# Kernel optimization log

Measured on AMD Instinct MI355X. Metric: run time of the kernel, lower is better.

## Reference

```python
import jax, jax.numpy as jnp
import numpy as np

B, D, NT, NZ = 16384, 64, 128, 2048


def setup_inputs() -> dict:
    key = jax.random.key(0)
    ks = jax.random.split(key, 5)
    return {
        "t": jax.random.uniform(ks[0], (1,), dtype=jnp.float32),
        "z": jax.random.normal(ks[1], (B, D), dtype=jnp.float32),
        "logp_z": jnp.zeros((B, 1), jnp.float32),
        "centres_z": jax.random.normal(ks[2], (NZ, D), dtype=jnp.float32),
        "log_sigmas_z": jnp.zeros((NZ,), jnp.float32),
        "centres_t": jax.random.normal(ks[3], (NT, 1), dtype=jnp.float32),
        "log_sigmas_t": jnp.zeros((NT,), jnp.float32),
        "W": 0.01 * jax.random.normal(ks[4], (D, NT, NZ + 1), dtype=jnp.float32),
    }


def _gauss(r):
    return jnp.exp(-r * r)


def _forward(t, z, centres_z, log_sigmas_z, centres_t, log_sigmas_t, W):
    # time RBF features Phi_t: (NT,)
    r_t = jnp.abs(t.reshape(1, 1) - centres_t.reshape(1, -1)) / jnp.exp(log_sigmas_t)
    phi_t = _gauss(r_t).reshape(-1)
    W_t = jnp.einsum('dij,i->dj', W, phi_t)  # (D, NZ+1)
    Wz, bias = W_t[:, :-1], W_t[:, -1]       # bias comes from the appended ones column
    # z RBF features via squared-distance identity (avoids [B,NZ,D] blowup)
    sq = (jnp.sum(z * z, axis=1, keepdims=True)
          + jnp.sum(centres_z * centres_z, axis=1)[None, :]
          - 2.0 * z @ centres_z.T)
    sq = jnp.maximum(sq, 0.0)                 # (B, NZ) squared distances
    inv_s2 = jnp.exp(-2.0 * log_sigmas_z)     # 1/sigma_j^2, (NZ,)
    phi_z = jnp.exp(-sq * inv_s2)             # gaussian(||z-c_j||/s_j), (B, NZ)
    dz_dt = phi_z @ Wz.T + bias               # (B, D)
    # exact Jacobian trace for gaussian basis:
    #   d phi_j / d z_i = -2 * phi_j * (z_i - c_{j,i}) / s_j^2
    #   tr(J)_b = sum_j phi_{b,j} * inv_s2_j * (-2) * (sum_i Wz[i,j] z_{b,i} - sum_i Wz[i,j] c_{j,i})
    q = jnp.einsum('dj,jd->j', Wz, centres_z)  # (NZ,)
    trace = -2.0 * jnp.sum(phi_z * inv_s2 * (z @ Wz - q), axis=1)  # (B,)
    dlogp_z_dt = -trace[:, None]               # (B, 1)
    return dz_dt, dlogp_z_dt


def reference(t, z, logp_z, centres_z, log_sigmas_z, centres_t, log_sigmas_t, W):
    return _forward(t, z, centres_z, log_sigmas_z, centres_t, log_sigmas_t, W)
```

## Files before the change

### kernel.cpp

```cpp
#include <hip/hip_runtime.h>
#include <math.h>

typedef unsigned int uint;
typedef unsigned short ushort;
typedef unsigned char uchar;
typedef unsigned long ulong_;
typedef __attribute__((ext_vector_type(4))) float f32x4;

#define BB  16384
#define DD  64
#define NT_ 128
#define NZ_ 2048
#define NJ_ 2049

#define BIAS_OFF 0
#define SCS_OFF  64
#define CZ8A_OFF 8256
#define CZ8B_OFF 24640
#define WZ8A_OFF 41024
#define WZ8B_OFF 57408
#define WZBP_OFF 73792
#define PART_OFF 106560

#if __has_builtin(__builtin_amdgcn_cvt_pk_fp8_f32)
__device__ __forceinline__ uint pk4_fp8(float a, float b, float c, float d) {
  int v = __builtin_amdgcn_cvt_pk_fp8_f32(a, b, 0, false);
  v = __builtin_amdgcn_cvt_pk_fp8_f32(c, d, v, true);
  return (uint)v;
}
__device__ __forceinline__ uchar f8_1(float x) {
  return (uchar)(__builtin_amdgcn_cvt_pk_fp8_f32(x, x, 0, false) & 0xFF);
}
#else
__device__ __forceinline__ uint sw_f8(float x) {
  uint u = __float_as_uint(x);
  uint s = (u >> 24) & 0x80u;
  float ax = __uint_as_float(u & 0x7FFFFFFFu);
  if (!(ax >= 0.015625f)) return s;
  if (ax >= 448.f) return s | 0x7Eu;
  uint q = __float_as_uint(ax);
  q += 0x7FFFFu + ((q >> 20) & 1u);
  uint e = (q >> 23) - 120u;
  return s | ((e & 0xFu) << 3) | ((q >> 20) & 7u);
}
__device__ __forceinline__ uchar f8_1(float x) { return (uchar)sw_f8(x); }
__device__ __forceinline__ uint pk4_fp8(float a, float b, float c, float d) {
  return sw_f8(a) | (sw_f8(b) << 8) | (sw_f8(c) << 16) | (sw_f8(d) << 24);
}
#endif

__global__ __launch_bounds__(256) void k_wt1(
    const float* __restrict__ t, const float* __restrict__ ct,
    const float* __restrict__ lst, const float* __restrict__ W,
    float* __restrict__ part)
{
  __shared__ float ph[32];
  int tx = threadIdx.x;
  int d  = blockIdx.y;
  int ic = blockIdx.z;
  if (tx < 32) {
    int i = ic * 32 + tx;
    float r = fabsf(t[0] - ct[i]) * __expf(-lst[i]);
    ph[tx] = __expf(-r * r);
  }
  __syncthreads();
  int j = blockIdx.x * 256 + tx;
  if (j >= NJ_) return;
  const float* Wp = W + (size_t)d * NT_ * NJ_ + (size_t)(ic * 32) * NJ_ + j;
  float acc = 0.f;
#pragma unroll
  for (int k = 0; k < 32; ++k) acc += Wp[(size_t)k * NJ_] * ph[k];
  part[((size_t)ic * 64 + d) * NJ_ + j] = acc;
}

__global__ __launch_bounds__(256) void k_prep2(
    const float* __restrict__ part, const float* __restrict__ cz,
    const float* __restrict__ lsz,
    float* __restrict__ bias, float4* __restrict__ scs,
    uchar* __restrict__ cz8a, uchar* __restrict__ cz8b,
    uchar* __restrict__ wz8a, uchar* __restrict__ wz8b,
    uchar* __restrict__ wzbp8)
{
  __shared__ float wt[64][9];
  int tid = threadIdx.x;
  int cb0 = blockIdx.x * 8;
#pragma unroll
  for (int h = 0; h < 2; ++h) {
    int f = h * 256 + tid;
    int d = f >> 3, c = f & 7;
    size_t idx = (size_t)d * NJ_ + cb0 + c;
    float s = part[idx] + part[(size_t)64 * NJ_ + idx]
            + part[(size_t)128 * NJ_ + idx] + part[(size_t)192 * NJ_ + idx];
    wt[d][c] = s;
    int cg = cb0 + c;
    wzbp8[((size_t)(cg >> 5) * 64 + d) * 32 + (cg & 31)] = f8_1(s);
  }
  if (blockIdx.x == 0 && tid < 64) {
    size_t idx = (size_t)tid * NJ_ + 2048;
    bias[tid] = part[idx] + part[(size_t)64 * NJ_ + idx]
              + part[(size_t)128 * NJ_ + idx] + part[(size_t)192 * NJ_ + idx];
  }
  __syncthreads();
  int cl = tid >> 5;
  int k  = tid & 31;
  int c  = cb0 + cl;
  float cv0 = cz[(size_t)c * DD + k];
  float cv1 = cz[(size_t)c * DD + 32 + k];
  cz8a[(size_t)c * 32 + k] = f8_1(cv0);
  cz8b[(size_t)c * 32 + k] = f8_1(cv1);
  float w0 = wt[k][cl], w1 = wt[32 + k][cl];
  wz8a[(size_t)c * 32 + k] = f8_1(w0);
  wz8b[(size_t)c * 32 + k] = f8_1(w1);
  float ca = cv0 * cv0 + cv1 * cv1;
  float qa = w0 * cv0 + w1 * cv1;
  qa += __shfl_xor(qa, 1);  ca += __shfl_xor(ca, 1);
  qa += __shfl_xor(qa, 2);  ca += __shfl_xor(ca, 2);
  qa += __shfl_xor(qa, 4);  ca += __shfl_xor(ca, 4);
  qa += __shfl_xor(qa, 8);  ca += __shfl_xor(ca, 8);
  qa += __shfl_xor(qa, 16); ca += __shfl_xor(ca, 16);
  if (k == 0) {
    float inv = __expf(-2.f * lsz[c]);
    scs[c] = make_float4(ca, inv, qa, inv * 1.44269504f);
  }
}

#define PH_LD 40

__global__ __launch_bounds__(256, 2) void k_fused(
    const float* __restrict__ z,
    const uchar* __restrict__ cz8a, const uchar* __restrict__ cz8b,
    const uchar* __restrict__ wz8a, const uchar* __restrict__ wz8b,
    const uchar* __restrict__ wzbp8,
    const float4* __restrict__ scs, const float* __restrict__ bias,
    float* __restrict__ out)
{
  __shared__ char smem[10240];
  __shared__ float dlr[4][32];
  uchar* phs = (uchar*)smem;
  float* eps = (float*)smem;

  int tid  = threadIdx.x;
  int ws   = tid >> 6;
  int lane = tid & 63;
  int lrow = lane & 15, quad = lane >> 4;
  int b0 = blockIdx.x * 32;

  long az[2][2];
  float zzr[2][4];
#pragma unroll
  for (int mt = 0; mt < 2; ++mt) {
    const float* zr = z + (size_t)(b0 + mt * 16 + lrow) * DD + quad * 8;
    float4 v0 = *(const float4*)zr;
    float4 v1 = *(const float4*)(zr + 4);
    float4 v2 = *(const float4*)(zr + 32);
    float4 v3 = *(const float4*)(zr + 36);
    uint l0 = pk4_fp8(v0.x, v0.y, v0.z, v0.w);
    uint l1 = pk4_fp8(v1.x, v1.y, v1.z, v1.w);
    uint h0 = pk4_fp8(v2.x, v2.y, v2.z, v2.w);
    uint h1 = pk4_fp8(v3.x, v3.y, v3.z, v3.w);
    az[mt][0] = (long)(((ulong_)l1 << 32) | l0);
    az[mt][1] = (long)(((ulong_)h1 << 32) | h0);
    float ss = v0.x * v0.x + v0.y * v0.y + v0.z * v0.z + v0.w * v0.w
             + v1.x * v1.x + v1.y * v1.y + v1.z * v1.z + v1.w * v1.w
             + v2.x * v2.x + v2.y * v2.y + v2.z * v2.z + v2.w * v2.w
             + v3.x * v3.x + v3.y * v3.y + v3.z * v3.z + v3.w * v3.w;
    ss += __shfl_xor(ss, 16);
    ss += __shfl_xor(ss, 32);
#pragma unroll
    for (int i = 0; i < 4; ++i) zzr[mt][i] = __shfl(ss, quad * 4 + i);
  }

  f32x4 acc[2][4];
#pragma unroll
  for (int mt = 0; mt < 2; ++mt)
#pragma unroll
    for (int nt = 0; nt < 4; ++nt) acc[mt][nt] = (f32x4){0.f, 0.f, 0.f, 0.f};
  float dl[2][4] = {{0.f}};

  const f32x4 zero = (f32x4){0.f, 0.f, 0.f, 0.f};
  int cbase = ws * 512;
  int pbase = ws * 32 * PH_LD;

  long Abc0[2][2], Abc1[2][2], Abw0[2][2], Abw1[2][2], Abb[2][4];
  float4 Asc[2][2];
#define LOADB(PAR, C0)                                                         \
  do {                                                                         \
    int c0_ = (C0);                                                            \
    _Pragma("unroll")                                                          \
    for (int nt = 0; nt < 2; ++nt) {                                           \
      int cg_ = c0_ + nt * 16 + lrow;                                          \
      size_t ro_ = (size_t)cg_ * 32 + quad * 8;                                \
      Abc0[PAR][nt] = *(const long*)(cz8a + ro_);                              \
      Abc1[PAR][nt] = *(const long*)(cz8b + ro_);                              \
      Abw0[PAR][nt] = *(const long*)(wz8a + ro_);                              \
      Abw1[PAR][nt] = *(const long*)(wz8b + ro_);                              \
      Asc[PAR][nt]  = scs[cg_];                                                \
    }                                                                          \
    size_t cb_ = (size_t)(c0_ >> 5) * 64 * 32;                                 \
    _Pragma("unroll")                                                          \
    for (int nt = 0; nt < 4; ++nt)                                             \
      Abb[PAR][nt] =                                                           \
          *(const long*)(wzbp8 + cb_ + (size_t)(nt * 16 + lrow) * 32 + quad * 8); \
  } while (0)

  LOADB(0, cbase);
#pragma unroll 2
  for (int it = 0; it < 16; ++it) {
    int par = it & 1;
    int pb = par * (4 * 32 * PH_LD) + pbase;

    f32x4 d1a[2][2], d2a[2][2];
#pragma unroll
    for (int nt = 0; nt < 2; ++nt)
#pragma unroll
      for (int mt = 0; mt < 2; ++mt) {
        f32x4 d1 = __builtin_amdgcn_mfma_f32_16x16x32_fp8_fp8(az[mt][0], Abc0[par][nt], zero, 0, 0, 0);
        d1       = __builtin_amdgcn_mfma_f32_16x16x32_fp8_fp8(az[mt][1], Abc1[par][nt], d1,   0, 0, 0);
        f32x4 d2 = __builtin_amdgcn_mfma_f32_16x16x32_fp8_fp8(az[mt][0], Abw0[par][nt], zero, 0, 0, 0);
        d2       = __builtin_amdgcn_mfma_f32_16x16x32_fp8_fp8(az[mt][1], Abw1[par][nt], d2,   0, 0, 0);
        d1a[nt][mt] = d1;
        d2a[nt][mt] = d2;
      }

    LOADB(par ^ 1, cbase + ((it + 1) & 15) * 32);

#pragma unroll
    for (int nt = 0; nt < 2; ++nt) {
      float4 sc = Asc[par][nt];
#pragma unroll
      for (int mt = 0; mt < 2; ++mt) {
#pragma unroll
        for (int i = 0; i < 4; ++i) {
          float e = fmaf(d1a[nt][mt][i], 2.f, -(zzr[mt][i] + sc.x)) * sc.w;
          e = fminf(e, 0.f);
          float p;
          asm("v_exp_f32 %0, %1" : "=v"(p) : "v"(e));
          dl[mt][i] += p * sc.y * (d2a[nt][mt][i] - sc.z);
          phs[pb + (mt * 16 + quad * 4 + i) * PH_LD + nt * 16 + lrow] = f8_1(p);
        }
      }
    }

    long ap0 = *(const long*)&phs[pb + lrow * PH_LD + quad * 8];
    long ap1 = *(const long*)&phs[pb + (16 + lrow) * PH_LD + quad * 8];
    __builtin_amdgcn_s_setprio(1);
#pragma unroll
    for (int nt = 0; nt < 4; ++nt) {
      acc[0][nt] = __builtin_amdgcn_mfma_f32_16x16x32_fp8_fp8(ap0, Abb[par][nt], acc[0][nt], 0, 0, 0);
      acc[1][nt] = __builtin_amdgcn_mfma_f32_16x16x32_fp8_fp8(ap1, Abb[par][nt], acc[1][nt], 0, 0, 0);
    }
    __builtin_amdgcn_s_setprio(0);
  }
#undef LOADB

#pragma unroll
  for (int mt = 0; mt < 2; ++mt)
#pragma unroll
    for (int i = 0; i < 4; ++i) {
      float v = dl[mt][i];
      v += __shfl_xor(v, 1);
      v += __shfl_xor(v, 2);
      v += __shfl_xor(v, 4);
      v += __shfl_xor(v, 8);
      if (lrow == 0) dlr[ws][mt * 16 + quad * 4 + i] = v;
    }

  for (int s = 0; s < 4; ++s) {
    __syncthreads();
    if (ws == s) {
#pragma unroll
      for (int mt = 0; mt < 2; ++mt)
#pragma unroll
        for (int nt = 0; nt < 4; ++nt)
#pragma unroll
          for (int i = 0; i < 4; ++i) {
            int r = mt * 16 + quad * 4 + i;
            int d = nt * 16 + lrow;
            if (s == 0) eps[r * 68 + d] = acc[mt][nt][i];
            else        eps[r * 68 + d] += acc[mt][nt][i];
          }
    }
  }
  __syncthreads();

  {
    int r = tid >> 3, d0 = (tid & 7) * 8;
    float4 e0 = *(const float4*)&eps[r * 68 + d0];
    float4 e1 = *(const float4*)&eps[r * 68 + d0 + 4];
    float4 bv0 = *(const float4*)&bias[d0];
    float4 bv1 = *(const float4*)&bias[d0 + 4];
    float4 o0, o1;
    o0.x = e0.x + bv0.x; o0.y = e0.y + bv0.y; o0.z = e0.z + bv0.z; o0.w = e0.w + bv0.w;
    o1.x = e1.x + bv1.x; o1.y = e1.y + bv1.y; o1.z = e1.z + bv1.z; o1.w = e1.w + bv1.w;
    *(float4*)&out[(size_t)(b0 + r) * DD + d0]     = o0;
    *(float4*)&out[(size_t)(b0 + r) * DD + d0 + 4] = o1;
  }
  if (tid < 32) {
    float s = dlr[0][tid] + dlr[1][tid] + dlr[2][tid] + dlr[3][tid];
    out[(size_t)BB * DD + b0 + tid] = 2.f * s;
  }
}

extern "C" void kernel_launch(void* const* d_in, const int* in_sizes, int n_in,
                              void* d_out, int out_size, void* d_ws, size_t ws_size,
                              hipStream_t stream)
{
  const float* t   = (const float*)d_in[0];
  const float* z   = (const float*)d_in[1];
  const float* cz  = (const float*)d_in[3];
  const float* lsz = (const float*)d_in[4];
  const float* ct  = (const float*)d_in[5];
  const float* lst = (const float*)d_in[6];
  const float* W   = (const float*)d_in[7];
  float* out = (float*)d_out;
  float* ws  = (float*)d_ws;

  float*  bias = ws + BIAS_OFF;
  float4* scs  = (float4*)(ws + SCS_OFF);
  uchar*  cz8a = (uchar*)(ws + CZ8A_OFF);
  uchar*  cz8b = (uchar*)(ws + CZ8B_OFF);
  uchar*  wz8a = (uchar*)(ws + WZ8A_OFF);
  uchar*  wz8b = (uchar*)(ws + WZ8B_OFF);
  uchar*  wzbp8 = (uchar*)(ws + WZBP_OFF);
  float*  part = ws + PART_OFF;

  k_wt1<<<dim3(9, 64, 4), 256, 0, stream>>>(t, ct, lst, W, part);
  k_prep2<<<dim3(256), 256, 0, stream>>>(part, cz, lsz, bias, scs,
                                         cz8a, cz8b, wz8a, wz8b, wzbp8);
  k_fused<<<dim3(BB / 32), 256, 0, stream>>>(z, cz8a, cz8b,
                                             wz8a, wz8b, wzbp8, scs, bias, out);
}
```

Measured before the change: 137.8 us.

## Transpose MFMA operands so phi stays in registers, replacing LDS staging with shuffles

The first-stage MFMAs now take the centre/weight tiles as the A operand and z as B, so each lane's results run along centres for a single batch row. The fp8 phi tile for the second MFMA is then built from packed registers with cross-lane shuffles instead of being written to and read back from shared memory. Per-centre constants are split into separate float arrays, loaded as float4 along the centre axis and pre-folded (−c²·il2, −inv·q), which trims the per-element arithmetic and the trace reduction. The cost is extra shuffle and select instructions plus three global float4 loads per iteration.

```diff
diff --git a/kernel.cpp b/kernel.cpp
--- a/kernel.cpp
+++ b/kernel.cpp
@@ -14,13 +14,15 @@
 #define NJ_ 2049
 
 #define BIAS_OFF 0
-#define SCS_OFF  64
-#define CZ8A_OFF 8256
-#define CZ8B_OFF 24640
-#define WZ8A_OFF 41024
-#define WZ8B_OFF 57408
-#define WZBP_OFF 73792
-#define PART_OFF 106560
+#define IL2_OFF  64
+#define A0_OFF   2112
+#define NIQ_OFF  4160
+#define CZ8A_OFF 6208
+#define CZ8B_OFF 22592
+#define WZ8A_OFF 38976
+#define WZ8B_OFF 55360
+#define WZBP_OFF 71744
+#define PART_OFF 104512
 
 #if __has_builtin(__builtin_amdgcn_cvt_pk_fp8_f32)
 __device__ __forceinline__ uint pk4_fp8(float a, float b, float c, float d) {
@@ -76,7 +78,8 @@
 __global__ __launch_bounds__(256) void k_prep2(
     const float* __restrict__ part, const float* __restrict__ cz,
     const float* __restrict__ lsz,
-    float* __restrict__ bias, float4* __restrict__ scs,
+    float* __restrict__ bias,
+    float* __restrict__ il2a, float* __restrict__ a0a, float* __restrict__ niqa,
     uchar* __restrict__ cz8a, uchar* __restrict__ cz8b,
     uchar* __restrict__ wz8a, uchar* __restrict__ wz8b,
     uchar* __restrict__ wzbp8)
@@ -120,24 +123,24 @@
   qa += __shfl_xor(qa, 16); ca += __shfl_xor(ca, 16);
   if (k == 0) {
     float inv = __expf(-2.f * lsz[c]);
-    scs[c] = make_float4(ca, inv, qa, inv * 1.44269504f);
-  }
-}
-
-#define PH_LD 40
+    float il2 = inv * 1.44269504f;
+    il2a[c] = il2;
+    a0a[c]  = -ca * il2;
+    niqa[c] = -inv * qa;
+  }
+}
 
 __global__ __launch_bounds__(256, 2) void k_fused(
     const float* __restrict__ z,
     const uchar* __restrict__ cz8a, const uchar* __restrict__ cz8b,
     const uchar* __restrict__ wz8a, const uchar* __restrict__ wz8b,
     const uchar* __restrict__ wzbp8,
-    const float4* __restrict__ scs, const float* __restrict__ bias,
-    float* __restrict__ out)
+    const float* __restrict__ il2a, const float* __restrict__ a0a,
+    const float* __restrict__ niqa,
+    const float* __restrict__ bias, float* __restrict__ out)
 {
-  __shared__ char smem[10240];
+  __shared__ float eps[32 * 68];
   __shared__ float dlr[4][32];
-  uchar* phs = (uchar*)smem;
-  float* eps = (float*)smem;
 
   int tid  = threadIdx.x;
   int ws   = tid >> 6;
@@ -146,7 +149,7 @@
   int b0 = blockIdx.x * 32;
 
   long az[2][2];
-  float zzr[2][4];
+  float nzz[2];
 #pragma unroll
   for (int mt = 0; mt < 2; ++mt) {
     const float* zr = z + (size_t)(b0 + mt * 16 + lrow) * DD + quad * 8;
@@ -166,8 +169,7 @@
              + v3.x * v3.x + v3.y * v3.y + v3.z * v3.z + v3.w * v3.w;
     ss += __shfl_xor(ss, 16);
     ss += __shfl_xor(ss, 32);
-#pragma unroll
-    for (int i = 0; i < 4; ++i) zzr[mt][i] = __shfl(ss, quad * 4 + i);
+    nzz[mt] = -ss;
   }
 
   f32x4 acc[2][4];
@@ -175,14 +177,12 @@
   for (int mt = 0; mt < 2; ++mt)
 #pragma unroll
     for (int nt = 0; nt < 4; ++nt) acc[mt][nt] = (f32x4){0.f, 0.f, 0.f, 0.f};
-  float dl[2][4] = {{0.f}};
+  float dl[2] = {0.f, 0.f};
 
   const f32x4 zero = (f32x4){0.f, 0.f, 0.f, 0.f};
   int cbase = ws * 512;
-  int pbase = ws * 32 * PH_LD;
 
   long Abc0[2][2], Abc1[2][2], Abw0[2][2], Abw1[2][2], Abb[2][4];
-  float4 Asc[2][2];
 #define LOADB(PAR, C0)                                                         \
   do {                                                                         \
     int c0_ = (C0);                                                            \
@@ -194,7 +194,6 @@
       Abc1[PAR][nt] = *(const long*)(cz8b + ro_);                              \
       Abw0[PAR][nt] = *(const long*)(wz8a + ro_);                              \
       Abw1[PAR][nt] = *(const long*)(wz8b + ro_);                              \
-      Asc[PAR][nt]  = scs[cg_];                                                \
     }                                                                          \
     size_t cb_ = (size_t)(c0_ >> 5) * 64 * 32;                                 \
     _Pragma("unroll")                                                          \
@@ -207,42 +206,67 @@
 #pragma unroll 2
   for (int it = 0; it < 16; ++it) {
     int par = it & 1;
-    int pb = par * (4 * 32 * PH_LD) + pbase;
+    int c0  = cbase + it * 32;
+
+    float4 ilv[2], a0v[2], nqv[2];
+#pragma unroll
+    for (int nt = 0; nt < 2; ++nt) {
+      int cb = c0 + nt * 16 + quad * 4;
+      ilv[nt] = *(const float4*)&il2a[cb];
+      a0v[nt] = *(const float4*)&a0a[cb];
+      nqv[nt] = *(const float4*)&niqa[cb];
+    }
 
     f32x4 d1a[2][2], d2a[2][2];
 #pragma unroll
     for (int nt = 0; nt < 2; ++nt)
 #pragma unroll
       for (int mt = 0; mt < 2; ++mt) {
-        f32x4 d1 = __builtin_amdgcn_mfma_f32_16x16x32_fp8_fp8(az[mt][0], Abc0[par][nt], zero, 0, 0, 0);
-        d1       = __builtin_amdgcn_mfma_f32_16x16x32_fp8_fp8(az[mt][1], Abc1[par][nt], d1,   0, 0, 0);
-        f32x4 d2 = __builtin_amdgcn_mfma_f32_16x16x32_fp8_fp8(az[mt][0], Abw0[par][nt], zero, 0, 0, 0);
-        d2       = __builtin_amdgcn_mfma_f32_16x16x32_fp8_fp8(az[mt][1], Abw1[par][nt], d2,   0, 0, 0);
+        f32x4 d1 = __builtin_amdgcn_mfma_f32_16x16x32_fp8_fp8(Abc0[par][nt], az[mt][0], zero, 0, 0, 0);
+        d1       = __builtin_amdgcn_mfma_f32_16x16x32_fp8_fp8(Abc1[par][nt], az[mt][1], d1,   0, 0, 0);
+        f32x4 d2 = __builtin_amdgcn_mfma_f32_16x16x32_fp8_fp8(Abw0[par][nt], az[mt][0], zero, 0, 0, 0);
+        d2       = __builtin_amdgcn_mfma_f32_16x16x32_fp8_fp8(Abw1[par][nt], az[mt][1], d2,   0, 0, 0);
         d1a[nt][mt] = d1;
         d2a[nt][mt] = d2;
       }
 
     LOADB(par ^ 1, cbase + ((it + 1) & 15) * 32);
 
-#pragma unroll
-    for (int nt = 0; nt < 2; ++nt) {
-      float4 sc = Asc[par][nt];
-#pragma unroll
-      for (int mt = 0; mt < 2; ++mt) {
+    uint u00, u01, u10, u11;
+#pragma unroll
+    for (int mt = 0; mt < 2; ++mt)
+#pragma unroll
+      for (int nt = 0; nt < 2; ++nt) {
+        float pv[4];
 #pragma unroll
         for (int i = 0; i < 4; ++i) {
-          float e = fmaf(d1a[nt][mt][i], 2.f, -(zzr[mt][i] + sc.x)) * sc.w;
+          float il2 = ilv[nt][i];
+          float t2  = d1a[nt][mt][i] + d1a[nt][mt][i];
+          float uu  = fmaf(il2, nzz[mt], a0v[nt][i]);
+          float e   = fmaf(t2, il2, uu);
           e = fminf(e, 0.f);
           float p;
           asm("v_exp_f32 %0, %1" : "=v"(p) : "v"(e));
-          dl[mt][i] += p * sc.y * (d2a[nt][mt][i] - sc.z);
-          phs[pb + (mt * 16 + quad * 4 + i) * PH_LD + nt * 16 + lrow] = f8_1(p);
+          float g = fmaf(d2a[nt][mt][i] * 0.69314718f, il2, nqv[nt][i]);
+          dl[mt] = fmaf(p, g, dl[mt]);
+          pv[i] = p;
         }
+        uint uv = pk4_fp8(pv[0], pv[1], pv[2], pv[3]);
+        if (mt == 0) { if (nt == 0) u00 = uv; else u01 = uv; }
+        else         { if (nt == 0) u10 = uv; else u11 = uv; }
       }
-    }
-
-    long ap0 = *(const long*)&phs[pb + lrow * PH_LD + quad * 8];
-    long ap1 = *(const long*)&phs[pb + (16 + lrow) * PH_LD + quad * 8];
+
+    int  sl = lrow + ((lane & 16) << 1);
+    bool hh = lane >= 32;
+    uint l0a = __shfl(u00, sl),      l1a = __shfl(u01, sl);
+    uint h0a = __shfl(u00, sl + 16), h1a = __shfl(u01, sl + 16);
+    uint lo0 = hh ? l1a : l0a,       hi0 = hh ? h1a : h0a;
+    long ap0 = (long)(((ulong_)hi0 << 32) | lo0);
+    uint l0b = __shfl(u10, sl),      l1b = __shfl(u11, sl);
+    uint h0b = __shfl(u10, sl + 16), h1b = __shfl(u11, sl + 16);
+    uint lo1 = hh ? l1b : l0b,       hi1 = hh ? h1b : h0b;
+    long ap1 = (long)(((ulong_)hi1 << 32) | lo1);
+
     __builtin_amdgcn_s_setprio(1);
 #pragma unroll
     for (int nt = 0; nt < 4; ++nt) {
@@ -254,16 +278,12 @@
 #undef LOADB
 
 #pragma unroll
-  for (int mt = 0; mt < 2; ++mt)
-#pragma unroll
-    for (int i = 0; i < 4; ++i) {
-      float v = dl[mt][i];
-      v += __shfl_xor(v, 1);
-      v += __shfl_xor(v, 2);
-      v += __shfl_xor(v, 4);
-      v += __shfl_xor(v, 8);
-      if (lrow == 0) dlr[ws][mt * 16 + quad * 4 + i] = v;
-    }
+  for (int mt = 0; mt < 2; ++mt) {
+    float v = dl[mt];
+    v += __shfl_xor(v, 16);
+    v += __shfl_xor(v, 32);
+    if (quad == 0) dlr[ws][mt * 16 + lrow] = v;
+  }
 
   for (int s = 0; s < 4; ++s) {
     __syncthreads();
@@ -316,7 +336,9 @@
   float* ws  = (float*)d_ws;
 
   float*  bias = ws + BIAS_OFF;
-  float4* scs  = (float4*)(ws + SCS_OFF);
+  float*  il2a = ws + IL2_OFF;
+  float*  a0a  = ws + A0_OFF;
+  float*  niqa = ws + NIQ_OFF;
   uchar*  cz8a = (uchar*)(ws + CZ8A_OFF);
   uchar*  cz8b = (uchar*)(ws + CZ8B_OFF);
   uchar*  wz8a = (uchar*)(ws + WZ8A_OFF);
@@ -325,8 +347,10 @@
   float*  part = ws + PART_OFF;
 
   k_wt1<<<dim3(9, 64, 4), 256, 0, stream>>>(t, ct, lst, W, part);
-  k_prep2<<<dim3(256), 256, 0, stream>>>(part, cz, lsz, bias, scs,
+  k_prep2<<<dim3(256), 256, 0, stream>>>(part, cz, lsz, bias,
+                                         il2a, a0a, niqa,
                                          cz8a, cz8b, wz8a, wz8b, wzbp8);
   k_fused<<<dim3(BB / 32), 256, 0, stream>>>(z, cz8a, cz8b,
-                                             wz8a, wz8b, wzbp8, scs, bias, out);
-}
+                                             wz8a, wz8b, wzbp8,
+                                             il2a, a0a, niqa, bias, out);
+}
```

Result: no change. 137.5 us (-0.2%).
